# Optimization experiments

Hardware: AMD Instinct MI355X
Metric: run time of the kernel (lower is better)

Reference implementation:

```python
import jax, jax.numpy as jnp
import numpy as np

B, N, D_IN = 64, 512, 768
FEA, HEADS = 256, 8
NEG_SLOPE = 0.2  # GATConv default leaky_relu slope


def setup_inputs() -> dict:
    key = jax.random.key(0)
    ks = jax.random.split(key, 7)
    scale = lambda fan_in: 1.0 / np.sqrt(fan_in)
    return {
        "x": jax.random.normal(ks[0], (B, N, D_IN), dtype=jnp.float32),
        # outer LazyLinear(fea_dim) with bias
        "W1": jax.random.normal(ks[1], (D_IN, FEA), dtype=jnp.float32) * scale(D_IN),
        "b1": jnp.zeros((FEA,), dtype=jnp.float32),
        # GATConv lin: Linear(FEA, HEADS*FEA, bias=False)
        "Wg": jax.random.normal(ks[2], (FEA, HEADS * FEA), dtype=jnp.float32) * scale(FEA),
        "att_src": jax.random.normal(ks[3], (HEADS, FEA), dtype=jnp.float32) * scale(FEA),
        "att_dst": jax.random.normal(ks[4], (HEADS, FEA), dtype=jnp.float32) * scale(FEA),
        # GATConv bias (concat=False -> out_channels)
        "bias_g": jnp.zeros((FEA,), dtype=jnp.float32),
    }


def reference(x, W1, b1, Wg, att_src, att_dst, bias_g):
    # outer projection: [B,N,FEA]
    x1 = jnp.einsum("bnd,df->bnf", x, W1) + b1
    # GAT projection into heads: [B,N,H,C]
    h = jnp.einsum("bnf,fk->bnk", x1, Wg).reshape(B, N, HEADS, FEA)
    # per-node attention logits: [B,N,H]
    a_src = jnp.einsum("bnhc,hc->bnh", h, att_src)
    a_dst = jnp.einsum("bnhc,hc->bnh", h, att_dst)
    # graph is fully connected + self-loops (PyG add_self_loops=True),
    # so per-target softmax == dense softmax over all source nodes j.
    # logits[b,h,i,j] = a_dst[b,i,h] + a_src[b,j,h]
    logits = a_dst.transpose(0, 2, 1)[:, :, :, None] + a_src.transpose(0, 2, 1)[:, :, None, :]
    logits = jnp.where(logits >= 0, logits, NEG_SLOPE * logits)  # leaky_relu
    alpha = jax.nn.softmax(logits, axis=-1)  # [B,H,I,J]
    # weighted aggregation: out[b,i,h,c] = sum_j alpha[b,h,i,j] * h[b,j,h,c]
    out = jnp.einsum("bhij,bjhc->bihc", alpha, h)
    out = out.mean(axis=2) + bias_g  # concat=False -> mean over heads, [B,N,FEA]
    return out.mean(axis=1)  # mean over nodes -> [B,FEA]
```

## Files before the change

kernel.cpp:

```cpp
#include <hip/hip_runtime.h>

#define BATCH 64
#define NNODE 512
#define D_IN 768
#define FEA 256
#define HEADS 8
#define M_ROWS (BATCH * NNODE)
#define NEG_SLOPE 0.2f
#define LOG2E 1.4426950408889634f

typedef __attribute__((ext_vector_type(4))) float f32x4;
typedef __attribute__((ext_vector_type(8))) short bf16x8;

__device__ __forceinline__ ushort f2bf(float f) {
    union { float f; unsigned u; } v; v.f = f;
    unsigned r = v.u + 0x7fffu + ((v.u >> 16) & 1u);
    return (ushort)(r >> 16);
}
__device__ __forceinline__ float exp2fast(float v) { return __builtin_amdgcn_exp2f(v); }

__global__ __launch_bounds__(256) void k_att_proj(const float* __restrict__ Wg,
                                                  const float* __restrict__ att_src,
                                                  const float* __restrict__ att_dst,
                                                  float* __restrict__ was,
                                                  float* __restrict__ wad) {
    int h = blockIdx.x;
    int f = threadIdx.x;
    const float* a = (blockIdx.y == 0) ? att_src : att_dst;
    float* o = (blockIdx.y == 0) ? was : wad;
    const float* wrow = Wg + (size_t)f * (HEADS * FEA) + h * FEA;
    const float* av = a + h * FEA;
    float acc = 0.f;
    #pragma unroll 4
    for (int c = 0; c < FEA; c++) acc += wrow[c] * av[c];
    o[h * FEA + f] = acc;
}

__global__ __launch_bounds__(256) void k_prep_was1(const float* __restrict__ W1,
                                                   const float* __restrict__ b1,
                                                   const float* __restrict__ was,
                                                   const float* __restrict__ wad,
                                                   ushort* __restrict__ Bpk,
                                                   float* __restrict__ c_sd) {
    __shared__ float wvl[16 * 260];
    int t = threadIdx.x;
    int kt = blockIdx.x;
    for (int sIdx = t; sIdx < 4096; sIdx += 256) {
        int col = sIdx >> 8, f = sIdx & 255;
        wvl[col * 260 + f] = (col < 8) ? was[col * 256 + f] : wad[(col - 8) * 256 + f];
    }
    __syncthreads();
    int kl = t >> 4, col = t & 15;
    #pragma unroll
    for (int half = 0; half < 2; half++) {
        int kloc = kl + half * 16;
        int k = kt * 32 + kloc;
        const float* wrow = W1 + (size_t)k * 256;
        float acc = 0.f;
        #pragma unroll 4
        for (int f0 = 0; f0 < 256; f0 += 4) {
            float4 a4 = *(const float4*)&wrow[f0];
            float4 v4 = *(const float4*)&wvl[col * 260 + f0];
            acc += a4.x * v4.x + a4.y * v4.y + a4.z * v4.z + a4.w * v4.w;
        }
        Bpk[kt * 1024 + ((kloc >> 3) * 16 + col) * 8 + (kloc & 7)] = f2bf(acc);
    }
    if (kt == 0 && t < 16) {
        float a = 0.f;
        for (int f = 0; f < 256; f++) a += b1[f] * wvl[t * 260 + f];
        c_sd[t] = a;
    }
}

__global__ __launch_bounds__(256) void k_logits(const float* __restrict__ x,
                                                const ushort* __restrict__ Bpk,
                                                const float* __restrict__ c_sd,
                                                float* __restrict__ a_src,
                                                float* __restrict__ a_dst) {
    int t = threadIdx.x;
    int w = t >> 6, l = t & 63;
    int lr = l & 15, lk = l >> 4;
    int row0w = blockIdx.x * 64 + w * 16;
    const float* ap = x + (size_t)(row0w + lr) * D_IN + lk * 8;
    const ushort* bp = Bpk + l * 8;

    f32x4 A0[3], A1[3];
    bf16x8 Bf[3];
    A0[0] = *(const f32x4*)(ap);      A1[0] = *(const f32x4*)(ap + 4);
    Bf[0] = *(const bf16x8*)(bp);
    A0[1] = *(const f32x4*)(ap + 32); A1[1] = *(const f32x4*)(ap + 36);
    Bf[1] = *(const bf16x8*)(bp + 1024);
    f32x4 acc = {};

    #pragma unroll
    for (int kt = 0; kt < 24; kt++) {
        int cur = kt % 3;
        if (kt + 2 < 24) {
            int nx = (kt + 2) % 3;
            A0[nx] = *(const f32x4*)(ap + (kt + 2) * 32);
            A1[nx] = *(const f32x4*)(ap + (kt + 2) * 32 + 4);
            Bf[nx] = *(const bf16x8*)(bp + (size_t)(kt + 2) * 1024);
        }
        bf16x8 af;
        af[0] = (short)f2bf(A0[cur].x); af[1] = (short)f2bf(A0[cur].y);
        af[2] = (short)f2bf(A0[cur].z); af[3] = (short)f2bf(A0[cur].w);
        af[4] = (short)f2bf(A1[cur].x); af[5] = (short)f2bf(A1[cur].y);
        af[6] = (short)f2bf(A1[cur].z); af[7] = (short)f2bf(A1[cur].w);
        acc = __builtin_amdgcn_mfma_f32_16x16x32_bf16(af, Bf[cur], acc, 0, 0, 0);
    }
    int col = lr;
    float cadd = c_sd[col];
    float* dst = (col < 8) ? a_src : a_dst;
    int h = col & 7;
    #pragma unroll
    for (int r = 0; r < 4; r++) {
        int rr = row0w + lk * 4 + r;
        int b = rr >> 9, n = rr & 511;
        dst[((size_t)(b * 8 + h) << 9) + n] = (acc[r] + cadd) * LOG2E;
    }
}

__global__ __launch_bounds__(512) void k_softmax(const float* __restrict__ a_src,
                                                 const float* __restrict__ a_dst,
                                                 float* __restrict__ wout,
                                                 float* __restrict__ s_w) {
    __shared__ float s_srt[512], d_srt[512];
    __shared__ float E1[512], E2[512], PA[512], PB[512];
    __shared__ float red[8], tA[8], tB[8];
    int t = threadIdx.x;
    int lane = t & 63, wv = t >> 6;
    int bh = blockIdx.x;
    float sv = a_src[((size_t)bh << 9) + t];
    float dv = a_dst[((size_t)bh << 9) + t];
    float v_s = sv, v_d = dv;
    float mx = sv;
    #pragma unroll
    for (int off = 32; off; off >>= 1) mx = fmaxf(mx, __shfl_xor(mx, off));
    if (lane == 0) red[wv] = mx;
    __syncthreads();
    mx = red[0];
    #pragma unroll
    for (int k = 1; k < 8; k++) mx = fmaxf(mx, red[k]);
    for (int k = 2; k <= 512; k <<= 1) {
        for (int j = k >> 1; j > 0; j >>= 1) {
            bool lower = ((t & j) == 0);
            bool tmin = (lower == ((t & k) == 0));
            if (j >= 64) {
                __syncthreads();
                s_srt[t] = v_s; d_srt[t] = v_d;
                __syncthreads();
                float ps = s_srt[t ^ j], pd = d_srt[t ^ j];
                v_s = tmin ? fminf(v_s, ps) : fmaxf(v_s, ps);
                v_d = tmin ? fminf(v_d, pd) : fmaxf(v_d, pd);
            } else {
                float ps = __shfl_xor(v_s, j);
                float pd = __shfl_xor(v_d, j);
                v_s = tmin ? fminf(v_s, ps) : fmaxf(v_s, ps);
                v_d = tmin ? fminf(v_d, pd) : fmaxf(v_d, pd);
            }
        }
    }
    __syncthreads();
    s_srt[t] = v_s; d_srt[t] = v_d;
    float e1 = exp2fast(v_s - mx);
    float e2 = exp2fast(0.2f * (v_s - mx));
    #pragma unroll
    for (int off = 1; off < 64; off <<= 1) {
        float u1 = __shfl_up(e1, off);
        float u2 = __shfl_up(e2, off);
        if (lane >= off) { e1 += u1; e2 += u2; }
    }
    if (lane == 63) { tA[wv] = e1; tB[wv] = e2; }
    __syncthreads();
    float pre1 = 0.f, pre2 = 0.f, tot1 = 0.f, tot2 = 0.f;
    #pragma unroll
    for (int k = 0; k < 8; k++) {
        float a = tA[k], b = tB[k];
        tot1 += a; tot2 += b;
        if (k < wv) { pre1 += a; pre2 += b; }
    }
    e1 += pre1; e2 += pre2;
    E1[t] = e1; E2[t] = e2;
    __syncthreads();
    float v = v_d + mx;
    float mi = fmaxf(v, NEG_SLOPE * v);
    float key = -v_d;
    int lo = 0, hi = 512;
    #pragma unroll
    for (int it = 0; it < 9; it++) {
        if (lo < hi) {
            int mid = (lo + hi) >> 1;
            if (s_srt[mid] < key) lo = mid + 1; else hi = mid;
        }
    }
    float e1pre = lo ? E1[lo - 1] : 0.f;
    float e2pre = lo ? E2[lo - 1] : 0.f;
    float ga = exp2fast(v - mi);
    float gb = exp2fast(0.2f * v - mi);
    float L = ga * (tot1 - e1pre) + gb * e2pre;
    float linv = 1.f / L;
    float pa = ga * linv, pb = gb * linv;
    #pragma unroll
    for (int off = 1; off < 64; off <<= 1) {
        float u1 = __shfl_up(pa, off);
        float u2 = __shfl_up(pb, off);
        if (lane >= off) { pa += u1; pb += u2; }
    }
    __syncthreads();
    if (lane == 63) { tA[wv] = pa; tB[wv] = pb; }
    __syncthreads();
    float prp1 = 0.f, prp2 = 0.f, totp1 = 0.f, totp2 = 0.f;
    #pragma unroll
    for (int k = 0; k < 8; k++) {
        float a = tA[k], b = tB[k];
        totp1 += a; totp2 += b;
        if (k < wv) { prp1 += a; prp2 += b; }
    }
    pa += prp1; pb += prp2;
    PA[t] = pa; PB[t] = pb;
    __syncthreads();
    float key2 = -sv;
    int lo2 = 0, hi2 = 512;
    #pragma unroll
    for (int it = 0; it < 9; it++) {
        if (lo2 < hi2) {
            int mid = (lo2 + hi2) >> 1;
            if (d_srt[mid] < key2) lo2 = mid + 1; else hi2 = mid;
        }
    }
    float papre = lo2 ? PA[lo2 - 1] : 0.f;
    float pbpre = lo2 ? PB[lo2 - 1] : 0.f;
    float e1j = exp2fast(sv - mx);
    float e2j = exp2fast(0.2f * (sv - mx));
    float wj = e1j * (totp1 - papre) + e2j * pbpre;
    wout[((size_t)bh << 9) + t] = wj;
    float ssum = wj;
    #pragma unroll
    for (int off = 32; off; off >>= 1) ssum += __shfl_xor(ssum, off);
    __syncthreads();
    if (lane == 0) red[wv] = ssum;
    __syncthreads();
    if (t == 0) {
        float a = 0.f;
        #pragma unroll
        for (int k = 0; k < 8; k++) a += red[k];
        s_w[bh] = a;
    }
}

__global__ __launch_bounds__(256) void k_zsum(const float* __restrict__ w,
                                              const float* __restrict__ x,
                                              float* __restrict__ z_part) {
    __shared__ float wl[512];
    int t = threadIdx.x;
    int b = blockIdx.x, jc = blockIdx.y;
    {
        int idx = t;
        wl[idx] = w[((size_t)(b * 8 + (idx >> 6)) << 9) + jc * 64 + (idx & 63)];
        idx = t + 256;
        wl[idx] = w[((size_t)(b * 8 + (idx >> 6)) << 9) + jc * 64 + (idx & 63)];
    }
    __syncthreads();
    float acc[8][3] = {};
    const float* xp = x + ((size_t)(b * 512 + jc * 64)) * D_IN + t;
    for (int j0 = 0; j0 < 64; j0 += 4) {
        float4 wq[8];
        #pragma unroll
        for (int h = 0; h < 8; h++) wq[h] = *(const float4*)&wl[h * 64 + j0];
        #pragma unroll
        for (int jj = 0; jj < 4; jj++) {
            float x0 = xp[(size_t)(j0 + jj) * D_IN];
            float x1 = xp[(size_t)(j0 + jj) * D_IN + 256];
            float x2 = xp[(size_t)(j0 + jj) * D_IN + 512];
            #pragma unroll
            for (int h = 0; h < 8; h++) {
                float wv = (jj == 0) ? wq[h].x : (jj == 1) ? wq[h].y : (jj == 2) ? wq[h].z : wq[h].w;
                acc[h][0] += wv * x0;
                acc[h][1] += wv * x1;
                acc[h][2] += wv * x2;
            }
        }
    }
    #pragma unroll
    for (int h = 0; h < 8; h++) {
        size_t base = ((size_t)((b * 8 + jc) * 8 + h)) * D_IN + t;
        z_part[base] = acc[h][0];
        z_part[base + 256] = acc[h][1];
        z_part[base + 512] = acc[h][2];
    }
}

__global__ __launch_bounds__(256) void k_y(const float* __restrict__ z_part,
                                           const float* __restrict__ W1,
                                           const float* __restrict__ b1,
                                           const float* __restrict__ s_w,
                                           float* __restrict__ y_part) {
    __shared__ float zl[8 * 196];
    int t = threadIdx.x;
    int b = blockIdx.x, ds = blockIdx.y;
    for (int sIdx = t; sIdx < 1536; sIdx += 256) {
        int k = sIdx / 192, dd = sIdx - k * 192;
        float v = 0.f;
        #pragma unroll
        for (int jc = 0; jc < 8; jc++)
            v += z_part[((size_t)((b * 8 + jc) * 8 + k)) * D_IN + ds * 192 + dd];
        zl[k * 196 + dd] = v;
    }
    __syncthreads();
    float acc[8] = {};
    for (int dq = 0; dq < 48; dq++) {
        int dbase = ds * 192 + dq * 4;
        float w0 = W1[(size_t)(dbase + 0) * 256 + t];
        float w1 = W1[(size_t)(dbase + 1) * 256 + t];
        float w2 = W1[(size_t)(dbase + 2) * 256 + t];
        float w3 = W1[(size_t)(dbase + 3) * 256 + t];
        #pragma unroll
        for (int k = 0; k < 8; k++) {
            float4 zq = *(const float4*)&zl[k * 196 + dq * 4];
            acc[k] += zq.x * w0 + zq.y * w1 + zq.z * w2 + zq.w * w3;
        }
    }
    #pragma unroll
    for (int k = 0; k < 8; k++) {
        float v = acc[k];
        if (ds == 0) v += s_w[b * 8 + k] * b1[t];
        y_part[((size_t)ds * 512 + b * 8 + k) * 256 + t] = v;
    }
}

__global__ __launch_bounds__(256) void k_out(const float* __restrict__ y_part,
                                             const float* __restrict__ Wg,
                                             float* __restrict__ out_part) {
    __shared__ float Yl[64][16];
    int t = threadIdx.x;
    int h = blockIdx.x, fs = blockIdx.y, bq = blockIdx.z;
    int f0 = fs * 64, b0 = bq * 16;
    for (int sIdx = t; sIdx < 1024; sIdx += 256) {
        int bl = sIdx >> 6, fl = sIdx & 63;
        float v = 0.f;
        #pragma unroll
        for (int ds = 0; ds < 4; ds++)
            v += y_part[((size_t)(ds * 512) + (b0 + bl) * 8 + h) * 256 + f0 + fl];
        Yl[fl][bl] = v;
    }
    __syncthreads();
    float acc[16] = {};
    for (int fl = 0; fl < 64; fl++) {
        float wv = Wg[(size_t)(f0 + fl) * 2048 + h * 256 + t];
        #pragma unroll
        for (int bl = 0; bl < 16; bl++) acc[bl] += Yl[fl][bl] * wv;
    }
    #pragma unroll
    for (int bl = 0; bl < 16; bl++)
        out_part[((size_t)(h * 4 + fs) * 64 + b0 + bl) * 256 + t] = acc[bl];
}

__global__ __launch_bounds__(256) void k_out2(const float* __restrict__ out_part,
                                              const float* __restrict__ bias_g,
                                              float* __restrict__ out) {
    int t = threadIdx.x, b = blockIdx.x;
    float acc = 0.f;
    #pragma unroll
    for (int k = 0; k < 32; k++) acc += out_part[((size_t)k * 64 + b) * 256 + t];
    out[b * 256 + t] = bias_g[t] + acc * (1.f / 4096.f);
}

extern "C" void kernel_launch(void* const* d_in, const int* in_sizes, int n_in,
                              void* d_out, int out_size, void* d_ws, size_t ws_size,
                              hipStream_t stream) {
    const float* x       = (const float*)d_in[0];
    const float* W1      = (const float*)d_in[1];
    const float* b1      = (const float*)d_in[2];
    const float* Wg      = (const float*)d_in[3];
    const float* att_src = (const float*)d_in[4];
    const float* att_dst = (const float*)d_in[5];
    const float* bias_g  = (const float*)d_in[6];
    float* out = (float*)d_out;

    float* ws       = (float*)d_ws;
    float* was      = ws;
    float* wad      = ws + 2048;
    float* c_sd     = ws + 4096;
    ushort* Bpk     = (ushort*)(ws + 4112);
    float* a_src    = ws + 16400;
    float* a_dst    = ws + 278544;
    float* wsum     = ws + 540688;
    float* s_w      = ws + 802832;
    float* z_part   = ws + 803344;
    float* y_part   = ws + 3949072;
    float* out_part = ws + 4473360;

    k_att_proj<<<dim3(HEADS, 2), 256, 0, stream>>>(Wg, att_src, att_dst, was, wad);
    k_prep_was1<<<24, 256, 0, stream>>>(W1, b1, was, wad, Bpk, c_sd);
    k_logits<<<M_ROWS / 64, 256, 0, stream>>>(x, Bpk, c_sd, a_src, a_dst);
    k_softmax<<<BATCH * HEADS, 512, 0, stream>>>(a_src, a_dst, wsum, s_w);
    k_zsum<<<dim3(BATCH, 8), 256, 0, stream>>>(wsum, x, z_part);
    k_y<<<dim3(BATCH, 4), 256, 0, stream>>>(z_part, W1, b1, s_w, y_part);
    k_out<<<dim3(HEADS, 4, 4), 256, 0, stream>>>(y_part, Wg, out_part);
    k_out2<<<BATCH, 256, 0, stream>>>(out_part, bias_g, out);
}
```

Measured before the change: 100.4 us.

## Parallelize small prep kernels and split zsum into more vectorized chunks

The attention-projection kernel now uses a wave per output with coalesced float4 loads of Wg and a shuffle reduction, spread over four times as many blocks. The W1 prep kernel stages rows in LDS and splits each dot product across two halves, quadrupling its block count. The zsum kernel splits the node dimension into 16 chunks of 32 with float4 loads of x, giving twice as many blocks. The cost is a larger z_part buffer and more partial sums for k_y to reduce.

Result: faster. 94.40 us (-6.0%).

```diff
diff --git a/kernel.cpp b/kernel.cpp
--- a/kernel.cpp
+++ b/kernel.cpp
@@ -8,6 +8,7 @@
 #define M_ROWS (BATCH * NNODE)
 #define NEG_SLOPE 0.2f
 #define LOG2E 1.4426950408889634f
+#define JC 16
 
 typedef __attribute__((ext_vector_type(4))) float f32x4;
 typedef __attribute__((ext_vector_type(8))) short bf16x8;
@@ -25,15 +26,20 @@
                                                   float* __restrict__ was,
                                                   float* __restrict__ wad) {
     int h = blockIdx.x;
-    int f = threadIdx.x;
     const float* a = (blockIdx.y == 0) ? att_src : att_dst;
     float* o = (blockIdx.y == 0) ? was : wad;
-    const float* wrow = Wg + (size_t)f * (HEADS * FEA) + h * FEA;
-    const float* av = a + h * FEA;
-    float acc = 0.f;
-    #pragma unroll 4
-    for (int c = 0; c < FEA; c++) acc += wrow[c] * av[c];
-    o[h * FEA + f] = acc;
+    int wv = threadIdx.x >> 6, lane = threadIdx.x & 63;
+    float4 av = *(const float4*)&a[h * FEA + lane * 4];
+    int fbase = blockIdx.z * 64 + wv;
+    #pragma unroll
+    for (int i = 0; i < 16; i++) {
+        int f = fbase + i * 4;
+        float4 g = *(const float4*)&Wg[(size_t)f * (HEADS * FEA) + h * FEA + lane * 4];
+        float p = g.x * av.x + g.y * av.y + g.z * av.z + g.w * av.w;
+        #pragma unroll
+        for (int off = 32; off; off >>= 1) p += __shfl_xor(p, off);
+        if (lane == 0) o[h * FEA + f] = p;
+    }
 }
 
 __global__ __launch_bounds__(256) void k_prep_was1(const float* __restrict__ W1,
@@ -43,29 +49,39 @@
                                                    ushort* __restrict__ Bpk,
                                                    float* __restrict__ c_sd) {
     __shared__ float wvl[16 * 260];
-    int t = threadIdx.x;
-    int kt = blockIdx.x;
-    for (int sIdx = t; sIdx < 4096; sIdx += 256) {
-        int col = sIdx >> 8, f = sIdx & 255;
+    __shared__ float w1l[8][256];
+    __shared__ float partial[256];
+    int t = threadIdx.x;
+    int blk = blockIdx.x;
+    int k0 = blk * 8;
+    for (int i = t; i < 4096; i += 256) {
+        int col = i >> 8, f = i & 255;
         wvl[col * 260 + f] = (col < 8) ? was[col * 256 + f] : wad[(col - 8) * 256 + f];
     }
-    __syncthreads();
-    int kl = t >> 4, col = t & 15;
-    #pragma unroll
-    for (int half = 0; half < 2; half++) {
-        int kloc = kl + half * 16;
-        int k = kt * 32 + kloc;
-        const float* wrow = W1 + (size_t)k * 256;
-        float acc = 0.f;
-        #pragma unroll 4
-        for (int f0 = 0; f0 < 256; f0 += 4) {
-            float4 a4 = *(const float4*)&wrow[f0];
-            float4 v4 = *(const float4*)&wvl[col * 260 + f0];
-            acc += a4.x * v4.x + a4.y * v4.y + a4.z * v4.z + a4.w * v4.w;
-        }
-        Bpk[kt * 1024 + ((kloc >> 3) * 16 + col) * 8 + (kloc & 7)] = f2bf(acc);
-    }
-    if (kt == 0 && t < 16) {
+    for (int i = t; i < 2048; i += 256) {
+        int r = i >> 8, c = i & 255;
+        w1l[r][c] = W1[(size_t)(k0 + r) * 256 + c];
+    }
+    __syncthreads();
+    int col = t & 15, r = (t >> 4) & 7, half = t >> 7;
+    float acc = 0.f;
+    const float* wr = &w1l[r][half * 128];
+    const float* vr = &wvl[col * 260 + half * 128];
+    #pragma unroll 4
+    for (int f0 = 0; f0 < 128; f0 += 4) {
+        float4 a4 = *(const float4*)&wr[f0];
+        float4 v4 = *(const float4*)&vr[f0];
+        acc += a4.x * v4.x + a4.y * v4.y + a4.z * v4.z + a4.w * v4.w;
+    }
+    partial[t] = acc;
+    __syncthreads();
+    if (t < 128) {
+        float tot = partial[t] + partial[t + 128];
+        int kt = blk >> 2;
+        int kloc = (blk & 3) * 8 + r;
+        Bpk[kt * 1024 + ((kloc >> 3) * 16 + col) * 8 + (kloc & 7)] = f2bf(tot);
+    }
+    if (blk == 0 && t < 16) {
         float a = 0.f;
         for (int f = 0; f < 256; f++) a += b1[f] * wvl[t * 260 + f];
         c_sd[t] = a;
@@ -248,46 +264,30 @@
     }
 }
 
-__global__ __launch_bounds__(256) void k_zsum(const float* __restrict__ w,
+__global__ __launch_bounds__(192) void k_zsum(const float* __restrict__ w,
                                               const float* __restrict__ x,
                                               float* __restrict__ z_part) {
-    __shared__ float wl[512];
+    __shared__ float wl[256];
     int t = threadIdx.x;
     int b = blockIdx.x, jc = blockIdx.y;
-    {
-        int idx = t;
-        wl[idx] = w[((size_t)(b * 8 + (idx >> 6)) << 9) + jc * 64 + (idx & 63)];
-        idx = t + 256;
-        wl[idx] = w[((size_t)(b * 8 + (idx >> 6)) << 9) + jc * 64 + (idx & 63)];
-    }
-    __syncthreads();
-    float acc[8][3] = {};
-    const float* xp = x + ((size_t)(b * 512 + jc * 64)) * D_IN + t;
-    for (int j0 = 0; j0 < 64; j0 += 4) {
-        float4 wq[8];
-        #pragma unroll
-        for (int h = 0; h < 8; h++) wq[h] = *(const float4*)&wl[h * 64 + j0];
-        #pragma unroll
-        for (int jj = 0; jj < 4; jj++) {
-            float x0 = xp[(size_t)(j0 + jj) * D_IN];
-            float x1 = xp[(size_t)(j0 + jj) * D_IN + 256];
-            float x2 = xp[(size_t)(j0 + jj) * D_IN + 512];
-            #pragma unroll
-            for (int h = 0; h < 8; h++) {
-                float wv = (jj == 0) ? wq[h].x : (jj == 1) ? wq[h].y : (jj == 2) ? wq[h].z : wq[h].w;
-                acc[h][0] += wv * x0;
-                acc[h][1] += wv * x1;
-                acc[h][2] += wv * x2;
-            }
-        }
-    }
-    #pragma unroll
-    for (int h = 0; h < 8; h++) {
-        size_t base = ((size_t)((b * 8 + jc) * 8 + h)) * D_IN + t;
-        z_part[base] = acc[h][0];
-        z_part[base + 256] = acc[h][1];
-        z_part[base + 512] = acc[h][2];
-    }
+    for (int i = t; i < 256; i += 192) {
+        int h = i >> 5, j = i & 31;
+        wl[i] = w[((size_t)(b * 8 + h) << 9) + jc * 32 + j];
+    }
+    __syncthreads();
+    f32x4 acc[8] = {};
+    const float* xp = x + ((size_t)(b * 512 + jc * 32)) * D_IN + t * 4;
+    for (int j = 0; j < 32; j++) {
+        f32x4 xv = *(const f32x4*)(xp + (size_t)j * D_IN);
+        #pragma unroll
+        for (int h = 0; h < 8; h++) {
+            float wv = wl[h * 32 + j];
+            acc[h] = acc[h] + wv * xv;
+        }
+    }
+    #pragma unroll
+    for (int h = 0; h < 8; h++)
+        *(f32x4*)&z_part[((size_t)((b * JC + jc) * 8 + h)) * D_IN + t * 4] = acc[h];
 }
 
 __global__ __launch_bounds__(256) void k_y(const float* __restrict__ z_part,
@@ -302,8 +302,8 @@
         int k = sIdx / 192, dd = sIdx - k * 192;
         float v = 0.f;
         #pragma unroll
-        for (int jc = 0; jc < 8; jc++)
-            v += z_part[((size_t)((b * 8 + jc) * 8 + k)) * D_IN + ds * 192 + dd];
+        for (int jc = 0; jc < JC; jc++)
+            v += z_part[((size_t)((b * JC + jc) * 8 + k)) * D_IN + ds * 192 + dd];
         zl[k * 196 + dd] = v;
     }
     __syncthreads();
@@ -387,14 +387,14 @@
     float* wsum     = ws + 540688;
     float* s_w      = ws + 802832;
     float* z_part   = ws + 803344;
-    float* y_part   = ws + 3949072;
-    float* out_part = ws + 4473360;
-
-    k_att_proj<<<dim3(HEADS, 2), 256, 0, stream>>>(Wg, att_src, att_dst, was, wad);
-    k_prep_was1<<<24, 256, 0, stream>>>(W1, b1, was, wad, Bpk, c_sd);
+    float* y_part   = ws + 7094800;
+    float* out_part = ws + 7619088;
+
+    k_att_proj<<<dim3(HEADS, 2, 4), 256, 0, stream>>>(Wg, att_src, att_dst, was, wad);
+    k_prep_was1<<<96, 256, 0, stream>>>(W1, b1, was, wad, Bpk, c_sd);
     k_logits<<<M_ROWS / 64, 256, 0, stream>>>(x, Bpk, c_sd, a_src, a_dst);
     k_softmax<<<BATCH * HEADS, 512, 0, stream>>>(a_src, a_dst, wsum, s_w);
-    k_zsum<<<dim3(BATCH, 8), 256, 0, stream>>>(wsum, x, z_part);
+    k_zsum<<<dim3(BATCH, JC), 192, 0, stream>>>(wsum, x, z_part);
     k_y<<<dim3(BATCH, 4), 256, 0, stream>>>(z_part, W1, b1, s_w, y_part);
     k_out<<<dim3(HEADS, 4, 4), 256, 0, stream>>>(y_part, Wg, out_part);
     k_out2<<<BATCH, 256, 0, stream>>>(out_part, bias_g, out);
```
